# Optimization experiments

Hardware: AMD Instinct MI355X
Metric: run time of the kernel (lower is better)

Reference implementation:

```python
import jax, jax.numpy as jnp
import numpy as np

B, D = 500000, 3
EPS = 1e-8

def _matrix_sqrt_H(A):
    # Hermitian sqrt via eigh: Q diag((L^2)^0.25) Q^T  (matches torch code incl. |L| handling)
    L, Q = jnp.linalg.eigh(A)
    return jnp.einsum('bij,bj,bkj->bik', Q, (L ** 2) ** 0.25, Q)

def setup_inputs() -> dict:
    key = jax.random.key(0)
    k1, k2, k3, k4 = jax.random.split(key, 4)
    miu_1 = jax.random.normal(k1, (B, D), dtype=jnp.float32)
    miu_2 = jax.random.normal(k2, (B, D), dtype=jnp.float32)
    eye = jnp.eye(D, dtype=jnp.float32)
    M1 = jax.random.normal(k3, (B, D, D), dtype=jnp.float32)
    M2 = jax.random.normal(k4, (B, D, D), dtype=jnp.float32)
    # SPD covariances, as produced by a Gaussian-splatting pipeline
    cov_1 = 0.1 * jnp.einsum('bij,bkj->bik', M1, M1) + 1e-3 * eye
    cov_2 = 0.1 * jnp.einsum('bij,bkj->bik', M2, M2) + 1e-3 * eye
    return {"miu_1": miu_1, "miu_2": miu_2, "cov_1": cov_1, "cov_2": cov_2}

def reference(miu_1, miu_2, cov_1, cov_2):
    eye = jnp.eye(cov_1.shape[-1], dtype=cov_1.dtype)
    A_sqrt = _matrix_sqrt_H(cov_1 + eye * EPS)
    A_sqrt_inv = jnp.linalg.inv(A_sqrt + eye * EPS)
    C = jnp.einsum('bij,bjk,blk->bil', A_sqrt, cov_2, A_sqrt)  # A_sqrt cov_2 A_sqrt^T
    C_sqrt = _matrix_sqrt_H(C + eye * EPS)
    cov_velocity = jnp.einsum('bij,bjk,blk->bil', A_sqrt, C_sqrt, A_sqrt_inv)
    cov_velocity = cov_velocity + jnp.swapaxes(cov_velocity, -1, -2) - 2.0 * cov_1
    return (miu_2 - miu_1, cov_velocity)
```

## Files before the change

kernel.cpp:

```cpp
#include <hip/hip_runtime.h>
#include <math.h>

#define EPS 1e-8f

__device__ __forceinline__ void jangle(float app, float aqq, float apq,
                                       float &c, float &s, float &app2, float &aqq2) {
    float h     = aqq - app;
    float ah    = fabsf(h) + 1e-18f;
    float v     = apq + apq;
    float rad   = fmaf(ah, ah, v * v);
    float rr    = __builtin_amdgcn_rsqf(rad);
    float c2h   = fmaf(0.5f * ah, rr, 0.5f);
    float rc2   = __builtin_amdgcn_rsqf(c2h);
    c = c2h * rc2;
    float apq_s = (h < 0.0f) ? -apq : apq;
    s = apq_s * (rr * rc2);
    float dl    = copysignf(0.5f * (rad * rr - ah), h);
    app2 = app - dl;
    aqq2 = aqq + dl;
}

__device__ __forceinline__ void eigh3(
    float &a00, float &a01, float &a02, float &a11, float &a12, float &a22,
    float &q00, float &q01, float &q02,
    float &q10, float &q11, float &q12,
    float &q20, float &q21, float &q22)
{
    float c, s, x, y, t0, t1;
    jangle(a00, a11, a01, c, s, x, y); a00 = x; a11 = y; a01 = 0.0f;
    t0 = a02; t1 = a12; a02 = fmaf(c, t0, -s * t1); a12 = fmaf(c, t1, s * t0);
    q00 = c; q01 = s; q10 = -s; q11 = c;

    jangle(a00, a22, a02, c, s, x, y); a00 = x; a22 = y; a02 = 0.0f;
    t0 = a01; t1 = a12; a01 = fmaf(c, t0, -s * t1); a12 = fmaf(c, t1, s * t0);
    q02 = s * q00; q12 = s * q10; q20 = -s; q22 = c;
    q00 = c * q00; q10 = c * q10;

    jangle(a11, a22, a12, c, s, x, y); a11 = x; a22 = y; a12 = 0.0f;
    t0 = a01; t1 = a02; a01 = fmaf(c, t0, -s * t1); a02 = fmaf(c, t1, s * t0);
    t0 = q01; t1 = q02; q01 = fmaf(c, t0, -s * t1); q02 = fmaf(s, t0, c * t1);
    t0 = q11; t1 = q12; q11 = fmaf(c, t0, -s * t1); q12 = fmaf(s, t0, c * t1);
    q21 = -s * q22; q22 = c * q22;

    #pragma unroll
    for (int sw = 0; sw < 2; ++sw) {
        jangle(a00, a11, a01, c, s, x, y); a00 = x; a11 = y; a01 = 0.0f;
        t0 = a02; t1 = a12; a02 = fmaf(c, t0, -s * t1); a12 = fmaf(c, t1, s * t0);
        t0 = q00; t1 = q01; q00 = fmaf(c, t0, -s * t1); q01 = fmaf(s, t0, c * t1);
        t0 = q10; t1 = q11; q10 = fmaf(c, t0, -s * t1); q11 = fmaf(s, t0, c * t1);
        t0 = q20; t1 = q21; q20 = fmaf(c, t0, -s * t1); q21 = fmaf(s, t0, c * t1);

        jangle(a00, a22, a02, c, s, x, y); a00 = x; a22 = y; a02 = 0.0f;
        t0 = a01; t1 = a12; a01 = fmaf(c, t0, -s * t1); a12 = fmaf(c, t1, s * t0);
        t0 = q00; t1 = q02; q00 = fmaf(c, t0, -s * t1); q02 = fmaf(s, t0, c * t1);
        t0 = q10; t1 = q12; q10 = fmaf(c, t0, -s * t1); q12 = fmaf(s, t0, c * t1);
        t0 = q20; t1 = q22; q20 = fmaf(c, t0, -s * t1); q22 = fmaf(s, t0, c * t1);

        jangle(a11, a22, a12, c, s, x, y); a11 = x; a22 = y; a12 = 0.0f;
        t0 = a01; t1 = a02; a01 = fmaf(c, t0, -s * t1); a02 = fmaf(c, t1, s * t0);
        t0 = q01; t1 = q02; q01 = fmaf(c, t0, -s * t1); q02 = fmaf(s, t0, c * t1);
        t0 = q11; t1 = q12; q11 = fmaf(c, t0, -s * t1); q12 = fmaf(s, t0, c * t1);
        t0 = q21; t1 = q22; q21 = fmaf(c, t0, -s * t1); q22 = fmaf(s, t0, c * t1);
    }
}

__global__ __launch_bounds__(256, 7) void wasserstein_log_kernel(
    const float* __restrict__ miu1, const float* __restrict__ miu2,
    const float* __restrict__ cov1, const float* __restrict__ cov2,
    float* __restrict__ out, int B)
{
    int b = blockIdx.x * blockDim.x + threadIdx.x;
    if (b >= B) return;

    out[3*b + 0] = miu2[3*b + 0] - miu1[3*b + 0];
    out[3*b + 1] = miu2[3*b + 1] - miu1[3*b + 1];
    out[3*b + 2] = miu2[3*b + 2] - miu1[3*b + 2];

    const float* c1p = cov1 + 9*(size_t)b;
    const float* c2p = cov2 + 9*(size_t)b;
    float k00 = c1p[0], k01 = c1p[1], k02 = c1p[2],
          k11 = c1p[4], k12 = c1p[5], k22 = c1p[8];
    float m00 = c2p[0], m01 = c2p[1], m02 = c2p[2],
          m11 = c2p[4], m12 = c2p[5], m22 = c2p[8];

    float a00 = k00 + EPS, a01 = k01, a02 = k02,
          a11 = k11 + EPS, a12 = k12, a22 = k22 + EPS;
    float q00, q01, q02, q10, q11, q12, q20, q21, q22;
    eigh3(a00, a01, a02, a11, a12, a22,
          q00, q01, q02, q10, q11, q12, q20, q21, q22);

    float w0 = fmaxf(fabsf(a00), 1e-12f);
    float w1 = fmaxf(fabsf(a11), 1e-12f);
    float w2 = fmaxf(fabsf(a22), 1e-12f);
    float di0 = __builtin_amdgcn_rsqf(w0), di1 = __builtin_amdgcn_rsqf(w1),
          di2 = __builtin_amdgcn_rsqf(w2);
    float d0 = w0 * di0, d1 = w1 * di1, d2 = w2 * di2;

    float T00 = fmaf(m00, q00, fmaf(m01, q10, m02 * q20));
    float T01 = fmaf(m00, q01, fmaf(m01, q11, m02 * q21));
    float T02 = fmaf(m00, q02, fmaf(m01, q12, m02 * q22));
    float T10 = fmaf(m01, q00, fmaf(m11, q10, m12 * q20));
    float T11 = fmaf(m01, q01, fmaf(m11, q11, m12 * q21));
    float T12 = fmaf(m01, q02, fmaf(m11, q12, m12 * q22));
    float T20 = fmaf(m02, q00, fmaf(m12, q10, m22 * q20));
    float T21 = fmaf(m02, q01, fmaf(m12, q11, m22 * q21));
    float T22 = fmaf(m02, q02, fmaf(m12, q12, m22 * q22));

    float g00 = fmaf(q00, T00, fmaf(q10, T10, q20 * T20));
    float g01 = fmaf(q00, T01, fmaf(q10, T11, q20 * T21));
    float g02 = fmaf(q00, T02, fmaf(q10, T12, q20 * T22));
    float g11 = fmaf(q01, T01, fmaf(q11, T11, q21 * T21));
    float g12 = fmaf(q01, T02, fmaf(q11, T12, q21 * T22));
    float g22 = fmaf(q02, T02, fmaf(q12, T12, q22 * T22));

    float cp00 = fmaf(w0, g00, EPS);
    float cp11 = fmaf(w1, g11, EPS);
    float cp22 = fmaf(w2, g22, EPS);
    float cp01 = d0 * d1 * g01;
    float cp02 = d0 * d2 * g02;
    float cp12 = d1 * d2 * g12;

    float e00, e01, e02, e10, e11, e12, e20, e21, e22;
    eigh3(cp00, cp01, cp02, cp11, cp12, cp22,
          e00, e01, e02, e10, e11, e12, e20, e21, e22);
    float u0 = fmaxf(fabsf(cp00), 1e-12f);
    float u1 = fmaxf(fabsf(cp11), 1e-12f);
    float u2 = fmaxf(fabsf(cp22), 1e-12f);
    float ts0 = u0 * __builtin_amdgcn_rsqf(u0);
    float ts1 = u1 * __builtin_amdgcn_rsqf(u1);
    float ts2 = u2 * __builtin_amdgcn_rsqf(u2);

    float Ed00 = d0*e00, Ed01 = d0*e01, Ed02 = d0*e02;
    float Ed10 = d1*e10, Ed11 = d1*e11, Ed12 = d1*e12;
    float Ed20 = d2*e20, Ed21 = d2*e21, Ed22 = d2*e22;
    float Ei00 = di0*e00, Ei01 = di0*e01, Ei02 = di0*e02;
    float Ei10 = di1*e10, Ei11 = di1*e11, Ei12 = di1*e12;
    float Ei20 = di2*e20, Ei21 = di2*e21, Ei22 = di2*e22;

    float U00 = fmaf(q00, Ed00, fmaf(q01, Ed10, q02 * Ed20));
    float U01 = fmaf(q00, Ed01, fmaf(q01, Ed11, q02 * Ed21));
    float U02 = fmaf(q00, Ed02, fmaf(q01, Ed12, q02 * Ed22));
    float U10 = fmaf(q10, Ed00, fmaf(q11, Ed10, q12 * Ed20));
    float U11 = fmaf(q10, Ed01, fmaf(q11, Ed11, q12 * Ed21));
    float U12 = fmaf(q10, Ed02, fmaf(q11, Ed12, q12 * Ed22));
    float U20 = fmaf(q20, Ed00, fmaf(q21, Ed10, q22 * Ed20));
    float U21 = fmaf(q20, Ed01, fmaf(q21, Ed11, q22 * Ed21));
    float U22 = fmaf(q20, Ed02, fmaf(q21, Ed12, q22 * Ed22));

    float P00 = fmaf(q00, Ei00, fmaf(q01, Ei10, q02 * Ei20));
    float P01 = fmaf(q00, Ei01, fmaf(q01, Ei11, q02 * Ei21));
    float P02 = fmaf(q00, Ei02, fmaf(q01, Ei12, q02 * Ei22));
    float P10 = fmaf(q10, Ei00, fmaf(q11, Ei10, q12 * Ei20));
    float P11 = fmaf(q10, Ei01, fmaf(q11, Ei11, q12 * Ei21));
    float P12 = fmaf(q10, Ei02, fmaf(q11, Ei12, q12 * Ei22));
    float P20 = fmaf(q20, Ei00, fmaf(q21, Ei10, q22 * Ei20));
    float P21 = fmaf(q20, Ei01, fmaf(q21, Ei11, q22 * Ei21));
    float P22 = fmaf(q20, Ei02, fmaf(q21, Ei12, q22 * Ei22));

    float A0 = ts0 * U00, A1 = ts1 * U01, A2 = ts2 * U02;
    float B0 = ts0 * U10, B1 = ts1 * U11, B2 = ts2 * U12;
    float C0 = ts0 * U20, C1 = ts1 * U21, C2 = ts2 * U22;

    float W00 = 2.0f * fmaf(A0, P00, fmaf(A1, P01, A2 * P02));
    float W11 = 2.0f * fmaf(B0, P10, fmaf(B1, P11, B2 * P12));
    float W22 = 2.0f * fmaf(C0, P20, fmaf(C1, P21, C2 * P22));
    float W01 = fmaf(A0, P10, fmaf(A1, P11, fmaf(A2, P12,
                fmaf(B0, P00, fmaf(B1, P01, B2 * P02)))));
    float W02 = fmaf(A0, P20, fmaf(A1, P21, fmaf(A2, P22,
                fmaf(C0, P00, fmaf(C1, P01, C2 * P02)))));
    float W12 = fmaf(B0, P20, fmaf(B1, P21, fmaf(B2, P22,
                fmaf(C0, P10, fmaf(C1, P11, C2 * P12)))));

    float o00 = fmaf(-2.0f, k00, W00);
    float o01 = fmaf(-2.0f, k01, W01);
    float o02 = fmaf(-2.0f, k02, W02);
    float o11 = fmaf(-2.0f, k11, W11);
    float o12 = fmaf(-2.0f, k12, W12);
    float o22 = fmaf(-2.0f, k22, W22);

    float* oc = out + (size_t)3 * B + 9*(size_t)b;
    oc[0] = o00; oc[1] = o01; oc[2] = o02;
    oc[3] = o01; oc[4] = o11; oc[5] = o12;
    oc[6] = o02; oc[7] = o12; oc[8] = o22;
}

extern "C" void kernel_launch(void* const* d_in, const int* in_sizes, int n_in,
                              void* d_out, int out_size, void* d_ws, size_t ws_size,
                              hipStream_t stream) {
    const float* miu1 = (const float*)d_in[0];
    const float* miu2 = (const float*)d_in[1];
    const float* cov1 = (const float*)d_in[2];
    const float* cov2 = (const float*)d_in[3];
    float* out = (float*)d_out;
    int B = in_sizes[0] / 3;
    int threads = 256;
    int blocks = (B + threads - 1) / threads;
    hipLaunchKernelGGL(wasserstein_log_kernel, dim3(blocks), dim3(threads), 0, stream,
                       miu1, miu2, cov1, cov2, out, B);
}
```

Measured before the change: 97.61 us.

## Process two matrices per thread with vectorized 16-byte loads and stores

Each thread now handles a pair of adjacent batch elements, so the 18 contiguous floats per covariance pair can be read and written with float4/float2 vector accesses instead of scalar ones. The aim is to cut the number of memory instructions and improve coalescing on this bandwidth-heavy kernel. The occupancy hint of 7 waves is dropped from launch bounds. Exchanges: half as many threads, higher register pressure from two independent eigen-solves per thread, and a scalar tail path for odd B.

```diff
diff --git a/kernel.cpp b/kernel.cpp
--- a/kernel.cpp
+++ b/kernel.cpp
@@ -3,8 +3,11 @@
 
 #define EPS 1e-8f
 
-__device__ __forceinline__ void jangle(float app, float aqq, float apq,
-                                       float &c, float &s, float &app2, float &aqq2) {
+typedef float f4a __attribute__((ext_vector_type(4), aligned(4)));
+typedef float f2a __attribute__((ext_vector_type(2), aligned(4)));
+
+static __device__ __forceinline__ void jangle(float app, float aqq, float apq,
+                                              float &c, float &s, float &app2, float &aqq2) {
     float h     = aqq - app;
     float ah    = fabsf(h) + 1e-18f;
     float v     = apq + apq;
@@ -20,7 +23,7 @@
     aqq2 = aqq + dl;
 }
 
-__device__ __forceinline__ void eigh3(
+static __device__ __forceinline__ void eigh3(
     float &a00, float &a01, float &a02, float &a11, float &a12, float &a22,
     float &q00, float &q01, float &q02,
     float &q10, float &q11, float &q12,
@@ -64,25 +67,11 @@
     }
 }
 
-__global__ __launch_bounds__(256, 7) void wasserstein_log_kernel(
-    const float* __restrict__ miu1, const float* __restrict__ miu2,
-    const float* __restrict__ cov1, const float* __restrict__ cov2,
-    float* __restrict__ out, int B)
+static __device__ __forceinline__ void wlog_elem(
+    float k00, float k01, float k02, float k11, float k12, float k22,
+    float m00, float m01, float m02, float m11, float m12, float m22,
+    float &o00, float &o01, float &o02, float &o11, float &o12, float &o22)
 {
-    int b = blockIdx.x * blockDim.x + threadIdx.x;
-    if (b >= B) return;
-
-    out[3*b + 0] = miu2[3*b + 0] - miu1[3*b + 0];
-    out[3*b + 1] = miu2[3*b + 1] - miu1[3*b + 1];
-    out[3*b + 2] = miu2[3*b + 2] - miu1[3*b + 2];
-
-    const float* c1p = cov1 + 9*(size_t)b;
-    const float* c2p = cov2 + 9*(size_t)b;
-    float k00 = c1p[0], k01 = c1p[1], k02 = c1p[2],
-          k11 = c1p[4], k12 = c1p[5], k22 = c1p[8];
-    float m00 = c2p[0], m01 = c2p[1], m02 = c2p[2],
-          m11 = c2p[4], m12 = c2p[5], m22 = c2p[8];
-
     float a00 = k00 + EPS, a01 = k01, a02 = k02,
           a11 = k11 + EPS, a12 = k12, a22 = k22 + EPS;
     float q00, q01, q02, q10, q11, q12, q20, q21, q22;
@@ -171,17 +160,82 @@
     float W12 = fmaf(B0, P20, fmaf(B1, P21, fmaf(B2, P22,
                 fmaf(C0, P10, fmaf(C1, P11, C2 * P12)))));
 
-    float o00 = fmaf(-2.0f, k00, W00);
-    float o01 = fmaf(-2.0f, k01, W01);
-    float o02 = fmaf(-2.0f, k02, W02);
-    float o11 = fmaf(-2.0f, k11, W11);
-    float o12 = fmaf(-2.0f, k12, W12);
-    float o22 = fmaf(-2.0f, k22, W22);
-
-    float* oc = out + (size_t)3 * B + 9*(size_t)b;
-    oc[0] = o00; oc[1] = o01; oc[2] = o02;
-    oc[3] = o01; oc[4] = o11; oc[5] = o12;
-    oc[6] = o02; oc[7] = o12; oc[8] = o22;
+    o00 = fmaf(-2.0f, k00, W00);
+    o01 = fmaf(-2.0f, k01, W01);
+    o02 = fmaf(-2.0f, k02, W02);
+    o11 = fmaf(-2.0f, k11, W11);
+    o12 = fmaf(-2.0f, k12, W12);
+    o22 = fmaf(-2.0f, k22, W22);
+}
+
+__global__ __launch_bounds__(256) void wasserstein_log_kernel(
+    const float* __restrict__ miu1, const float* __restrict__ miu2,
+    const float* __restrict__ cov1, const float* __restrict__ cov2,
+    float* __restrict__ out, int B)
+{
+    int b0 = blockIdx.x * blockDim.x + threadIdx.x;
+    int nT = (B + 1) >> 1;
+    if (b0 >= nT) return;
+
+    if (2 * b0 + 1 < B) {
+        size_t cb = 18 * (size_t)b0;
+        const f4a* p1 = (const f4a*)(cov1 + cb);
+        f4a Pa0 = p1[0], Pa1 = p1[1], Pa2 = p1[2], Pa3 = p1[3];
+        f2a Pa4 = *(const f2a*)(cov1 + cb + 16);
+        const f4a* p2 = (const f4a*)(cov2 + cb);
+        f4a Pb0 = p2[0], Pb1 = p2[1], Pb2 = p2[2], Pb3 = p2[3];
+        f2a Pb4 = *(const f2a*)(cov2 + cb + 16);
+
+        size_t mb = 6 * (size_t)b0;
+        f4a M10 = *(const f4a*)(miu1 + mb);
+        f2a M11 = *(const f2a*)(miu1 + mb + 4);
+        f4a M20 = *(const f4a*)(miu2 + mb);
+        f2a M21 = *(const f2a*)(miu2 + mb + 4);
+
+        f4a UM; UM.x = M20.x - M10.x; UM.y = M20.y - M10.y;
+                UM.z = M20.z - M10.z; UM.w = M20.w - M10.w;
+        f2a UM2; UM2.x = M21.x - M11.x; UM2.y = M21.y - M11.y;
+        *(f4a*)(out + mb) = UM;
+        *(f2a*)(out + mb + 4) = UM2;
+
+        float oA00, oA01, oA02, oA11, oA12, oA22;
+        wlog_elem(Pa0.x, Pa0.y, Pa0.z, Pa1.x, Pa1.y, Pa2.x,
+                  Pb0.x, Pb0.y, Pb0.z, Pb1.x, Pb1.y, Pb2.x,
+                  oA00, oA01, oA02, oA11, oA12, oA22);
+        float oB00, oB01, oB02, oB11, oB12, oB22;
+        wlog_elem(Pa2.y, Pa2.z, Pa2.w, Pa3.y, Pa3.z, Pa4.y,
+                  Pb2.y, Pb2.z, Pb2.w, Pb3.y, Pb3.z, Pb4.y,
+                  oB00, oB01, oB02, oB11, oB12, oB22);
+
+        float* oc = out + 3 * (size_t)B + cb;
+        f4a S0; S0.x = oA00; S0.y = oA01; S0.z = oA02; S0.w = oA01;
+        f4a S1; S1.x = oA11; S1.y = oA12; S1.z = oA02; S1.w = oA12;
+        f4a S2; S2.x = oA22; S2.y = oB00; S2.z = oB01; S2.w = oB02;
+        f4a S3; S3.x = oB01; S3.y = oB11; S3.z = oB12; S3.w = oB02;
+        f2a S4; S4.x = oB12; S4.y = oB22;
+        ((f4a*)oc)[0] = S0; ((f4a*)oc)[1] = S1;
+        ((f4a*)oc)[2] = S2; ((f4a*)oc)[3] = S3;
+        *(f2a*)(oc + 16) = S4;
+    } else {
+        int b = B - 1;
+        size_t cb = 9 * (size_t)b;
+        float k00 = cov1[cb+0], k01 = cov1[cb+1], k02 = cov1[cb+2],
+              k11 = cov1[cb+4], k12 = cov1[cb+5], k22 = cov1[cb+8];
+        float m00 = cov2[cb+0], m01 = cov2[cb+1], m02 = cov2[cb+2],
+              m11 = cov2[cb+4], m12 = cov2[cb+5], m22 = cov2[cb+8];
+        size_t mbs = 3 * (size_t)b;
+        out[mbs+0] = miu2[mbs+0] - miu1[mbs+0];
+        out[mbs+1] = miu2[mbs+1] - miu1[mbs+1];
+        out[mbs+2] = miu2[mbs+2] - miu1[mbs+2];
+        float o00, o01, o02, o11, o12, o22;
+        wlog_elem(k00, k01, k02, k11, k12, k22,
+                  m00, m01, m02, m11, m12, m22,
+                  o00, o01, o02, o11, o12, o22);
+        float* oc = out + 3 * (size_t)B + cb;
+        oc[0] = o00; oc[1] = o01; oc[2] = o02;
+        oc[3] = o01; oc[4] = o11; oc[5] = o12;
+        oc[6] = o02; oc[7] = o12; oc[8] = o22;
+    }
 }
 
 extern "C" void kernel_launch(void* const* d_in, const int* in_sizes, int n_in,
@@ -192,9 +246,10 @@
     const float* cov1 = (const float*)d_in[2];
     const float* cov2 = (const float*)d_in[3];
     float* out = (float*)d_out;
-    int B = in_sizes[0] / 3;
+    int B  = in_sizes[0] / 3;
+    int nT = (B + 1) / 2;
     int threads = 256;
-    int blocks = (B + threads - 1) / threads;
+    int blocks = (nT + threads - 1) / threads;
     hipLaunchKernelGGL(wasserstein_log_kernel, dim3(blocks), dim3(threads), 0, stream,
                        miu1, miu2, cov1, cov2, out, B);
 }
```

New measurement: 99.61 us. 1.02x slower.
